# Performance work log

Hardware: AMD Instinct MI355X
Metric: run time of the kernel (lower is better)

Reference implementation:

```python
import jax, jax.numpy as jnp
import numpy as np

# Module hyperparameters (from init_kwargs)
HEAD_DIM = 64
PX = 16          # patches_x
PY = 16          # patches_y
FREQ_BASE = 100.0
FREQ_SCALE = 1.0


def _precompute_coeffs(positions):
    """RoPE cos/sin tables for one axis. feat_dim = HEAD_DIM // 2."""
    feat_dim = HEAD_DIM // 2          # each block-diagonal block is head_dim/2 wide
    num_freqs = feat_dim // 2         # rope splits block into (x, y) halves
    freqs = FREQ_SCALE * FREQ_BASE ** (-jnp.arange(num_freqs, dtype=jnp.float32) / num_freqs)
    angles = positions.astype(jnp.float32)[:, None] * freqs[None, :]   # [Sp, num_freqs]
    return jnp.cos(angles), jnp.sin(angles)


def _rope_apply(feats, cos, sin, inverse=False):
    """feats: [B, H, S, D] with D == 2*cos.shape[-1]; cos/sin: [Sp, D//2], tiled to S."""
    S = feats.shape[2]
    rep = S // cos.shape[0]           # tile per-image coeffs across cameras
    cos = jnp.tile(cos, (rep, 1))[None, None]   # [1,1,S,D//2]
    sin = jnp.tile(sin, (rep, 1))[None, None]
    d = feats.shape[-1] // 2
    x_in, y_in = feats[..., :d], feats[..., d:]
    if inverse:
        return jnp.concatenate([cos * x_in - sin * y_in, sin * x_in + cos * y_in], axis=-1)
    return jnp.concatenate([cos * x_in + sin * y_in, -sin * x_in + cos * y_in], axis=-1)


def _block_diag_rope(feats, cx, sx, cy, sy, inverse=False):
    """Block-diagonal: first head_dim//2 dims get x-axis RoPE, second half get y-axis RoPE."""
    h = feats.shape[-1] // 2
    return jnp.concatenate([
        _rope_apply(feats[..., :h], cx, sx, inverse),
        _rope_apply(feats[..., h:], cy, sy, inverse),
    ], axis=-1)


def setup_inputs() -> dict:
    key = jax.random.key(0)
    kq, kk, kv, kvm, kks = jax.random.split(key, 5)
    B, H, CAM = 2, 16, 8
    S = CAM * PX * PY   # 2048
    q = jax.random.normal(kq, (B, H, S, HEAD_DIM), dtype=jnp.float32)
    k = jax.random.normal(kk, (B, H, S, HEAD_DIM), dtype=jnp.float32)
    v = jax.random.normal(kv, (B, H, S, HEAD_DIM), dtype=jnp.float32)
    viewmats = jax.random.normal(kvm, (B, CAM, 4, 4), dtype=jnp.float32)
    Ks = jax.random.normal(kks, (B, CAM, 3, 3), dtype=jnp.float32)
    return {"q": q, "k": k, "v": v, "viewmats": viewmats, "Ks": Ks}


def reference(q, k, v, viewmats, Ks):
    # Per-image patch-grid positions, 'split' ordering: x fastest.
    pos_x = jnp.tile(jnp.arange(PX), PY)               # [PX*PY]
    pos_y = jnp.repeat(jnp.arange(PY), PX)             # [PX*PY]
    cx, sx = _precompute_coeffs(pos_x)
    cy, sy = _precompute_coeffs(pos_y)

    qe = _block_diag_rope(q, cx, sx, cy, sy)
    ke = _block_diag_rope(k, cx, sx, cy, sy)
    ve = _block_diag_rope(v, cx, sx, cy, sy)

    scale = 1.0 / jnp.sqrt(jnp.asarray(q.shape[-1], dtype=q.dtype))
    logits = jnp.einsum('bhqd,bhkd->bhqk', qe, ke) * scale
    attn = jax.nn.softmax(logits, axis=-1)
    out = jnp.einsum('bhqk,bhkd->bhqd', attn, ve)

    # Inverse RoPE on the output (PRoPE epilogue).
    return _block_diag_rope(out, cx, sx, cy, sy, inverse=True)
```

## Files before the change

kernel.cpp:

```cpp
#include <hip/hip_runtime.h>
#include <stdint.h>
#include <math.h>

typedef __attribute__((ext_vector_type(8))) short bf16x8;
typedef __attribute__((ext_vector_type(16))) float f32x16;

#define S_LEN 2048
#define D_HEAD 64
#define NT 32
#define NT_HALF 16
#define TILE_USH 4096
#define SCALE_LOG2E 0.1803368801111204f
#define M_FIXED 16.0f

static __device__ __forceinline__ unsigned short f2bf(float f) {
    union { float f; uint32_t u; } v; v.f = f;
    return (unsigned short)((v.u + 0x7fffu + ((v.u >> 16) & 1u)) >> 16);
}
static __device__ __forceinline__ uint32_t cvtpk(float lo, float hi) {
    uint32_t r;
    asm("v_cvt_pk_bf16_f32 %0, %1, %2" : "=v"(r) : "v"(lo), "v"(hi));
    return r;
}
static __device__ __forceinline__ float exp2_fast(float x) {
    float r;
    asm("v_exp_f32 %0, %1" : "=v"(r) : "v"(x));
    return r;
}
static __device__ __forceinline__ void pswap(uint32_t& a, uint32_t& b) {
    asm("v_permlane32_swap_b32 %0, %1" : "+v"(a), "+v"(b));
}

static __device__ __forceinline__ void build_tables(float (*tc)[16][16], float (*ts)[16][16],
                                                    int tid, int nthr) {
    for (int e = tid; e < 512; e += nthr) {
        int axis = e >> 8, pp = (e >> 4) & 15, j = e & 15;
        float freq = powf(100.0f, -(float)j * (1.0f / 16.0f));
        float ang = (float)pp * freq;
        float sv, cv;
        sincosf(ang, &sv, &cv);
        tc[axis][pp][j] = cv;
        ts[axis][pp][j] = sv;
    }
}

static __device__ __forceinline__ void rope_chunk(const float* __restrict__ src, int row0, int r, int c,
                                                  const float (*tc)[16][16], const float (*ts)[16][16],
                                                  float* e1, float* e2) {
    int d0 = c * 4;
    int srow = row0 + r;
    const float* p = src + (size_t)srow * D_HEAD + d0;
    float4 xv = *(const float4*)p;
    float4 yv = *(const float4*)(p + 16);
    float xs[4] = {xv.x, xv.y, xv.z, xv.w};
    float ys[4] = {yv.x, yv.y, yv.z, yv.w};
    int pos = srow & 255;
    int axis = c >> 3;
    int pp = axis ? (pos >> 4) : (pos & 15);
    int jb = d0 & 15;
#pragma unroll
    for (int i = 0; i < 4; ++i) {
        float cc = tc[axis][pp][jb + i];
        float ss = ts[axis][pp][jb + i];
        e1[i] = cc * xs[i] + ss * ys[i];
        e2[i] = cc * ys[i] - ss * xs[i];
    }
}

__global__ __launch_bounds__(256) void xyrope_prep_kernel(
    const float* __restrict__ k, const float* __restrict__ v,
    unsigned short* __restrict__ kw, unsigned short* __restrict__ vtw) {
    __shared__ unsigned short Kt[64][72];
    __shared__ unsigned short Vt[64][72];
    __shared__ float tc[2][16][16], ts[2][16][16];
    int tid = threadIdx.x;
    build_tables(tc, ts, tid, 256);
    __syncthreads();

    int bid = blockIdx.x;
    int bh = bid >> 5, kt = bid & 31;
    const float* kh = k + (size_t)bh * S_LEN * D_HEAD;
    const float* vh = v + (size_t)bh * S_LEN * D_HEAD;
    unsigned short* kimg = kw + ((size_t)bh * NT + kt) * TILE_USH;
    unsigned short* vimg = vtw + ((size_t)bh * NT + kt) * TILE_USH;

#pragma unroll
    for (int half = 0; half < 2; ++half) {
        int r = (tid >> 3) + half * 32;
        int ci_ = tid & 7;
        int c = ci_ + ((ci_ >> 2) << 2);
        int d0 = c * 4;
        float e1[4], e2[4];
        rope_chunk(kh, kt * 64, r, c, tc, ts, e1, e2);
#pragma unroll
        for (int i = 0; i < 4; ++i) { Kt[r][d0 + i] = f2bf(e1[i]); Kt[r][d0 + 16 + i] = f2bf(e2[i]); }
        rope_chunk(vh, kt * 64, r, c, tc, ts, e1, e2);
#pragma unroll
        for (int i = 0; i < 4; ++i) { Vt[r][d0 + i] = f2bf(e1[i]); Vt[r][d0 + 16 + i] = f2bf(e2[i]); }
    }
    __syncthreads();

    int l = tid & 63, grp = tid >> 6;
#pragma unroll
    for (int half = 0; half < 2; ++half) {
        int ci = grp + half * 4;
        int mt = ci & 1, ks = ci >> 1;
        {
            int row = (l & 31) + 32 * mt;
            int d0 = (l >> 5) * 8 + 16 * ks;
            uint4 w = *(const uint4*)&Kt[row][d0];
            *(uint4*)(kimg + ci * 512 + l * 8) = w;
        }
        {
            int dcol = (l & 31) + 32 * mt;
            int k0 = (l >> 5) * 8 + 16 * ks;
            union { unsigned short u[8]; uint4 q; } ov;
#pragma unroll
            for (int j = 0; j < 8; ++j) ov.u[j] = Vt[k0 + j][dcol];
            *(uint4*)(vimg + ci * 512 + l * 8) = ov.q;
        }
    }
}

struct AttnSmem {
    union {
        struct {
            unsigned short Kb[2][2][TILE_USH];
            unsigned short Vb[2][2][TILE_USH];
        } b;
        float mrg[4][64][34];
    } u;
    float tc[2][16][16];
    float ts[2][16][16];
};

static __device__ __forceinline__ void gl16(const void* g, void* l) {
    __builtin_amdgcn_global_load_lds((const __attribute__((address_space(1))) unsigned int*)g,
                                     (__attribute__((address_space(3))) unsigned int*)l, 16, 0, 0);
}
static __device__ __forceinline__ void stage_tile(const unsigned short* img, unsigned short* dstbuf, int t256) {
    const char* src = (const char*)img + t256 * 16;
    char* dst = (char*)dstbuf + (t256 >> 6) * 1024;
    gl16(src, dst);
    gl16(src + 4096, dst + 4096);
}
static __device__ __forceinline__ bf16x8 frag_ld(const unsigned short* buf, int ci, int lane) {
    union { uint4 u; bf16x8 v; } c;
    c.u = *(const uint4*)(buf + ci * 512 + lane * 8);
    return c.v;
}

__global__ __launch_bounds__(512, 4) void xyrope_attn_kernel(
    const float* __restrict__ q, const unsigned short* __restrict__ kw,
    const unsigned short* __restrict__ vtw, float* __restrict__ out) {
    __shared__ AttnSmem sm;
    int tid = threadIdx.x, bid = blockIdx.x;

    int xcd = bid & 7, slot = bid >> 3;
    int bh = xcd * 4 + (slot >> 4);
    int qt = slot & 15;

    int grp = tid >> 8;
    int t256 = tid & 255;
    const unsigned short* kimg = kw + ((size_t)bh * NT + grp * NT_HALF) * TILE_USH;
    const unsigned short* vimg = vtw + ((size_t)bh * NT + grp * NT_HALF) * TILE_USH;

    build_tables(sm.tc, sm.ts, tid, 512);
    stage_tile(kimg, sm.u.b.Kb[grp][0], t256);
    stage_tile(vimg, sm.u.b.Vb[grp][0], t256);
    __syncthreads();

    int lane = tid & 63;
    int wave = (tid >> 6) & 3;
    int ql = lane & 31, h = lane >> 5;
    int qrow = qt * 128 + wave * 32 + ql;
    int pos = qrow & 255, px = pos & 15, py = pos >> 4;

    const float* qp = q + ((size_t)bh * S_LEN + qrow) * D_HEAD + h * 8;
    float e[4][8];
#pragma unroll
    for (int ck = 0; ck < 4; ++ck) {
        float4 a = *(const float4*)(qp + ck * 16);
        float4 b = *(const float4*)(qp + ck * 16 + 4);
        e[ck][0] = a.x; e[ck][1] = a.y; e[ck][2] = a.z; e[ck][3] = a.w;
        e[ck][4] = b.x; e[ck][5] = b.y; e[ck][6] = b.z; e[ck][7] = b.w;
    }
#pragma unroll
    for (int ax = 0; ax < 2; ++ax) {
        int pp = ax ? py : px;
#pragma unroll
        for (int i = 0; i < 8; ++i) {
            float cc = sm.tc[ax][pp][8 * h + i];
            float ss = sm.ts[ax][pp][8 * h + i];
            float x = e[ax * 2][i], y = e[ax * 2 + 1][i];
            e[ax * 2][i] = (cc * x + ss * y) * SCALE_LOG2E;
            e[ax * 2 + 1][i] = (cc * y - ss * x) * SCALE_LOG2E;
        }
    }
    bf16x8 bq[4];
#pragma unroll
    for (int ck = 0; ck < 4; ++ck) {
        union { uint32_t w[4]; bf16x8 v; } uu;
#pragma unroll
        for (int t = 0; t < 4; ++t) uu.w[t] = cvtpk(e[ck][2 * t], e[ck][2 * t + 1]);
        bq[ck] = uu.v;
    }

    float l_run = 0.0f;
    f32x16 o0 = {}, o1 = {};

    for (int t = 0; t < NT_HALF; ++t) {
        int cur = t & 1;
        if (t + 1 < NT_HALF) {
            stage_tile(kimg + (t + 1) * TILE_USH, sm.u.b.Kb[grp][cur ^ 1], t256);
            stage_tile(vimg + (t + 1) * TILE_USH, sm.u.b.Vb[grp][cur ^ 1], t256);
        }
        const unsigned short* Ks = sm.u.b.Kb[grp][cur];
        const unsigned short* Vs = sm.u.b.Vb[grp][cur];

        f32x16 s0 = {}, s1 = {};
        __builtin_amdgcn_s_setprio(1);
#pragma unroll
        for (int ks = 0; ks < 4; ++ks) {
            bf16x8 a0 = frag_ld(Ks, ks * 2 + 0, lane);
            bf16x8 a1 = frag_ld(Ks, ks * 2 + 1, lane);
            s0 = __builtin_amdgcn_mfma_f32_32x32x16_bf16(a0, bq[ks], s0, 0, 0, 0);
            s1 = __builtin_amdgcn_mfma_f32_32x32x16_bf16(a1, bq[ks], s1, 0, 0, 0);
        }
        __builtin_amdgcn_s_setprio(0);

#pragma unroll
        for (int r = 0; r < 16; ++r) {
            s0[r] = exp2_fast(s0[r] - M_FIXED);
            s1[r] = exp2_fast(s1[r] - M_FIXED);
        }

        uint32_t pk[16];
#pragma unroll
        for (int tt = 0; tt < 8; ++tt) {
            pk[tt] = cvtpk(s0[2 * tt], s0[2 * tt + 1]);
            pk[8 + tt] = cvtpk(s1[2 * tt], s1[2 * tt + 1]);
        }
        float a8[8];
#pragma unroll
        for (int i = 0; i < 8; ++i)
            a8[i] = (s0[i] + s0[i + 8]) + (s1[i] + s1[i + 8]);
        l_run += ((a8[0] + a8[1]) + (a8[2] + a8[3])) + ((a8[4] + a8[5]) + (a8[6] + a8[7]));

        __builtin_amdgcn_s_setprio(1);
#pragma unroll
        for (int ks = 0; ks < 4; ++ks) {
            uint32_t w0 = pk[4 * ks], w1 = pk[4 * ks + 1], w2 = pk[4 * ks + 2], w3 = pk[4 * ks + 3];
            pswap(w0, w2);
            pswap(w1, w3);
            union { uint32_t w[4]; bf16x8 v; } pb;
            pb.w[0] = w0; pb.w[1] = w1; pb.w[2] = w2; pb.w[3] = w3;
            bf16x8 v0 = frag_ld(Vs, ks * 2 + 0, lane);
            bf16x8 v1 = frag_ld(Vs, ks * 2 + 1, lane);
            o0 = __builtin_amdgcn_mfma_f32_32x32x16_bf16(v0, pb.v, o0, 0, 0, 0);
            o1 = __builtin_amdgcn_mfma_f32_32x32x16_bf16(v1, pb.v, o1, 0, 0, 0);
        }
        __builtin_amdgcn_s_setprio(0);
        __syncthreads();
    }

    float* pl = &sm.u.mrg[wave][lane][0];
    if (grp == 1) {
#pragma unroll
        for (int r = 0; r < 16; ++r) { pl[r] = o0[r]; pl[16 + r] = o1[r]; }
        pl[32] = l_run;
    }
    __syncthreads();
    if (grp == 0) {
        float lt = l_run + pl[32];
        lt += __shfl_xor(lt, 32);
        float inv_l = 1.0f / lt;
#pragma unroll
        for (int r = 0; r < 16; ++r) {
            o0[r] += pl[r];
            o1[r] += pl[16 + r];
        }

        float* orow = out + ((size_t)bh * S_LEN + qrow) * D_HEAD;
#pragma unroll
        for (int mt = 0; mt < 2; ++mt) {
            float oo[16];
#pragma unroll
            for (int r = 0; r < 16; ++r) oo[r] = mt ? o1[r] : o0[r];
            int pp = mt ? py : px;
            float res[16];
#pragma unroll
            for (int r = 0; r < 8; ++r) {
                int j = (r & 3) + 8 * (r >> 2) + 4 * h;
                float cc = sm.tc[mt][pp][j];
                float ss = sm.ts[mt][pp][j];
                float x = oo[r] * inv_l, y = oo[r + 8] * inv_l;
                res[r] = cc * x - ss * y;
                res[r + 8] = ss * x + cc * y;
            }
#pragma unroll
            for (int gq = 0; gq < 4; ++gq) {
                float4 w = {res[gq * 4 + 0], res[gq * 4 + 1], res[gq * 4 + 2], res[gq * 4 + 3]};
                *(float4*)(orow + mt * 32 + gq * 8 + 4 * h) = w;
            }
        }
    }
}

extern "C" void kernel_launch(void* const* d_in, const int* in_sizes, int n_in,
                              void* d_out, int out_size, void* d_ws, size_t ws_size,
                              hipStream_t stream) {
    const float* q = (const float*)d_in[0];
    const float* k = (const float*)d_in[1];
    const float* v = (const float*)d_in[2];
    float* out = (float*)d_out;
    unsigned short* kw = (unsigned short*)d_ws;
    unsigned short* vtw = kw + (size_t)32 * NT * TILE_USH;
    hipLaunchKernelGGL(xyrope_prep_kernel, dim3(1024), dim3(256), 0, stream, k, v, kw, vtw);
    hipLaunchKernelGGL(xyrope_attn_kernel, dim3(512), dim3(512), 0, stream, q, kw, vtw, out);
}
```

Measured before the change: 64.99 us.

## Split key sequence across four wave groups with 32-key tiles and 1024-thread blocks

Re-layouts the prepared K and V^T images into 32-key tiles and raises the attention block to 1024 threads, so four wave groups each process a quarter of the keys instead of two groups processing halves. Each iteration now does half the MFMA work per tile, with smaller LDS staging. Partial outputs and row sums are reduced serially through shared memory across the four groups. The aim is more waves in flight to hide latency, at the cost of more barriers, a longer merge epilogue and more loop overhead per key.

```diff
diff --git a/kernel.cpp b/kernel.cpp
--- a/kernel.cpp
+++ b/kernel.cpp
@@ -7,9 +7,9 @@
 
 #define S_LEN 2048
 #define D_HEAD 64
-#define NT 32
-#define NT_HALF 16
-#define TILE_USH 4096
+#define NTILE 64
+#define TPG 16
+#define T32_USH 2048
 #define SCALE_LOG2E 0.1803368801111204f
 #define M_FIXED 16.0f
 
@@ -81,8 +81,8 @@
     int bh = bid >> 5, kt = bid & 31;
     const float* kh = k + (size_t)bh * S_LEN * D_HEAD;
     const float* vh = v + (size_t)bh * S_LEN * D_HEAD;
-    unsigned short* kimg = kw + ((size_t)bh * NT + kt) * TILE_USH;
-    unsigned short* vimg = vtw + ((size_t)bh * NT + kt) * TILE_USH;
+    unsigned short* kimg = kw + ((size_t)bh * NTILE + kt * 2) * T32_USH;
+    unsigned short* vimg = vtw + ((size_t)bh * NTILE + kt * 2) * T32_USH;
 
 #pragma unroll
     for (int half = 0; half < 2; ++half) {
@@ -100,24 +100,27 @@
     }
     __syncthreads();
 
-    int l = tid & 63, grp = tid >> 6;
-#pragma unroll
-    for (int half = 0; half < 2; ++half) {
-        int ci = grp + half * 4;
-        int mt = ci & 1, ks = ci >> 1;
+    int l = tid & 63;
+#pragma unroll
+    for (int pass = 0; pass < 2; ++pass) {
+        int g = pass * 4 + (tid >> 6);
+        int sub = g >> 2;
         {
-            int row = (l & 31) + 32 * mt;
-            int d0 = (l >> 5) * 8 + 16 * ks;
+            int ks = g & 3;
+            int row = sub * 32 + (l & 31);
+            int d0 = ks * 16 + (l >> 5) * 8;
             uint4 w = *(const uint4*)&Kt[row][d0];
-            *(uint4*)(kimg + ci * 512 + l * 8) = w;
+            *(uint4*)(kimg + (size_t)sub * T32_USH + ks * 512 + l * 8) = w;
         }
         {
+            int ci = g & 3;
+            int ks2 = ci >> 1, mt = ci & 1;
+            int k0 = sub * 32 + ks2 * 16 + (l >> 5) * 8;
             int dcol = (l & 31) + 32 * mt;
-            int k0 = (l >> 5) * 8 + 16 * ks;
             union { unsigned short u[8]; uint4 q; } ov;
 #pragma unroll
             for (int j = 0; j < 8; ++j) ov.u[j] = Vt[k0 + j][dcol];
-            *(uint4*)(vimg + ci * 512 + l * 8) = ov.q;
+            *(uint4*)(vimg + (size_t)sub * T32_USH + ci * 512 + l * 8) = ov.q;
         }
     }
 }
@@ -125,8 +128,8 @@
 struct AttnSmem {
     union {
         struct {
-            unsigned short Kb[2][2][TILE_USH];
-            unsigned short Vb[2][2][TILE_USH];
+            unsigned short Kb[4][2][T32_USH];
+            unsigned short Vb[4][2][T32_USH];
         } b;
         float mrg[4][64][34];
     } u;
@@ -142,7 +145,6 @@
     const char* src = (const char*)img + t256 * 16;
     char* dst = (char*)dstbuf + (t256 >> 6) * 1024;
     gl16(src, dst);
-    gl16(src + 4096, dst + 4096);
 }
 static __device__ __forceinline__ bf16x8 frag_ld(const unsigned short* buf, int ci, int lane) {
     union { uint4 u; bf16x8 v; } c;
@@ -150,7 +152,7 @@
     return c.v;
 }
 
-__global__ __launch_bounds__(512, 4) void xyrope_attn_kernel(
+__global__ __launch_bounds__(1024, 8) void xyrope_attn_kernel(
     const float* __restrict__ q, const unsigned short* __restrict__ kw,
     const unsigned short* __restrict__ vtw, float* __restrict__ out) {
     __shared__ AttnSmem sm;
@@ -162,18 +164,18 @@
 
     int grp = tid >> 8;
     int t256 = tid & 255;
-    const unsigned short* kimg = kw + ((size_t)bh * NT + grp * NT_HALF) * TILE_USH;
-    const unsigned short* vimg = vtw + ((size_t)bh * NT + grp * NT_HALF) * TILE_USH;
-
-    build_tables(sm.tc, sm.ts, tid, 512);
+    const unsigned short* kimg = kw + ((size_t)bh * NTILE + grp * TPG) * T32_USH;
+    const unsigned short* vimg = vtw + ((size_t)bh * NTILE + grp * TPG) * T32_USH;
+
+    build_tables(sm.tc, sm.ts, tid, 1024);
     stage_tile(kimg, sm.u.b.Kb[grp][0], t256);
     stage_tile(vimg, sm.u.b.Vb[grp][0], t256);
     __syncthreads();
 
     int lane = tid & 63;
-    int wave = (tid >> 6) & 3;
+    int qwave = (tid >> 6) & 3;
     int ql = lane & 31, h = lane >> 5;
-    int qrow = qt * 128 + wave * 32 + ql;
+    int qrow = qt * 128 + qwave * 32 + ql;
     int pos = qrow & 255, px = pos & 15, py = pos >> 4;
 
     const float* qp = q + ((size_t)bh * S_LEN + qrow) * D_HEAD + h * 8;
@@ -209,54 +211,45 @@
     float l_run = 0.0f;
     f32x16 o0 = {}, o1 = {};
 
-    for (int t = 0; t < NT_HALF; ++t) {
+    for (int t = 0; t < TPG; ++t) {
         int cur = t & 1;
-        if (t + 1 < NT_HALF) {
-            stage_tile(kimg + (t + 1) * TILE_USH, sm.u.b.Kb[grp][cur ^ 1], t256);
-            stage_tile(vimg + (t + 1) * TILE_USH, sm.u.b.Vb[grp][cur ^ 1], t256);
+        if (t + 1 < TPG) {
+            stage_tile(kimg + (t + 1) * T32_USH, sm.u.b.Kb[grp][cur ^ 1], t256);
+            stage_tile(vimg + (t + 1) * T32_USH, sm.u.b.Vb[grp][cur ^ 1], t256);
         }
         const unsigned short* Ks = sm.u.b.Kb[grp][cur];
         const unsigned short* Vs = sm.u.b.Vb[grp][cur];
 
-        f32x16 s0 = {}, s1 = {};
+        f32x16 s0 = {};
         __builtin_amdgcn_s_setprio(1);
 #pragma unroll
         for (int ks = 0; ks < 4; ++ks) {
-            bf16x8 a0 = frag_ld(Ks, ks * 2 + 0, lane);
-            bf16x8 a1 = frag_ld(Ks, ks * 2 + 1, lane);
+            bf16x8 a0 = frag_ld(Ks, ks, lane);
             s0 = __builtin_amdgcn_mfma_f32_32x32x16_bf16(a0, bq[ks], s0, 0, 0, 0);
-            s1 = __builtin_amdgcn_mfma_f32_32x32x16_bf16(a1, bq[ks], s1, 0, 0, 0);
         }
         __builtin_amdgcn_s_setprio(0);
 
 #pragma unroll
-        for (int r = 0; r < 16; ++r) {
-            s0[r] = exp2_fast(s0[r] - M_FIXED);
-            s1[r] = exp2_fast(s1[r] - M_FIXED);
-        }
-
-        uint32_t pk[16];
-#pragma unroll
-        for (int tt = 0; tt < 8; ++tt) {
-            pk[tt] = cvtpk(s0[2 * tt], s0[2 * tt + 1]);
-            pk[8 + tt] = cvtpk(s1[2 * tt], s1[2 * tt + 1]);
-        }
-        float a8[8];
-#pragma unroll
-        for (int i = 0; i < 8; ++i)
-            a8[i] = (s0[i] + s0[i + 8]) + (s1[i] + s1[i + 8]);
-        l_run += ((a8[0] + a8[1]) + (a8[2] + a8[3])) + ((a8[4] + a8[5]) + (a8[6] + a8[7]));
+        for (int r = 0; r < 16; ++r) s0[r] = exp2_fast(s0[r] - M_FIXED);
+
+        uint32_t pk[8];
+#pragma unroll
+        for (int tt = 0; tt < 8; ++tt) pk[tt] = cvtpk(s0[2 * tt], s0[2 * tt + 1]);
+        float a4[4];
+#pragma unroll
+        for (int i = 0; i < 4; ++i) a4[i] = (s0[i] + s0[i + 4]) + (s0[i + 8] + s0[i + 12]);
+        l_run += (a4[0] + a4[1]) + (a4[2] + a4[3]);
 
         __builtin_amdgcn_s_setprio(1);
 #pragma unroll
-        for (int ks = 0; ks < 4; ++ks) {
-            uint32_t w0 = pk[4 * ks], w1 = pk[4 * ks + 1], w2 = pk[4 * ks + 2], w3 = pk[4 * ks + 3];
+        for (int ks2 = 0; ks2 < 2; ++ks2) {
+            uint32_t w0 = pk[4 * ks2], w1 = pk[4 * ks2 + 1], w2 = pk[4 * ks2 + 2], w3 = pk[4 * ks2 + 3];
             pswap(w0, w2);
             pswap(w1, w3);
             union { uint32_t w[4]; bf16x8 v; } pb;
             pb.w[0] = w0; pb.w[1] = w1; pb.w[2] = w2; pb.w[3] = w3;
-            bf16x8 v0 = frag_ld(Vs, ks * 2 + 0, lane);
-            bf16x8 v1 = frag_ld(Vs, ks * 2 + 1, lane);
+            bf16x8 v0 = frag_ld(Vs, ks2 * 2 + 0, lane);
+            bf16x8 v1 = frag_ld(Vs, ks2 * 2 + 1, lane);
             o0 = __builtin_amdgcn_mfma_f32_32x32x16_bf16(v0, pb.v, o0, 0, 0, 0);
             o1 = __builtin_amdgcn_mfma_f32_32x32x16_bf16(v1, pb.v, o1, 0, 0, 0);
         }
@@ -264,11 +257,23 @@
         __syncthreads();
     }
 
-    float* pl = &sm.u.mrg[wave][lane][0];
-    if (grp == 1) {
+    float* pl = &sm.u.mrg[qwave][lane][0];
+    if (grp == 3) {
 #pragma unroll
         for (int r = 0; r < 16; ++r) { pl[r] = o0[r]; pl[16 + r] = o1[r]; }
         pl[32] = l_run;
+    }
+    __syncthreads();
+    if (grp == 2) {
+#pragma unroll
+        for (int r = 0; r < 16; ++r) { pl[r] += o0[r]; pl[16 + r] += o1[r]; }
+        pl[32] += l_run;
+    }
+    __syncthreads();
+    if (grp == 1) {
+#pragma unroll
+        for (int r = 0; r < 16; ++r) { pl[r] += o0[r]; pl[16 + r] += o1[r]; }
+        pl[32] += l_run;
     }
     __syncthreads();
     if (grp == 0) {
@@ -315,7 +320,7 @@
     const float* v = (const float*)d_in[2];
     float* out = (float*)d_out;
     unsigned short* kw = (unsigned short*)d_ws;
-    unsigned short* vtw = kw + (size_t)32 * NT * TILE_USH;
+    unsigned short* vtw = kw + (size_t)32 * NTILE * T32_USH;
     hipLaunchKernelGGL(xyrope_prep_kernel, dim3(1024), dim3(256), 0, stream, k, v, kw, vtw);
-    hipLaunchKernelGGL(xyrope_attn_kernel, dim3(512), dim3(512), 0, stream, q, kw, vtw, out);
-}
+    hipLaunchKernelGGL(xyrope_attn_kernel, dim3(512), dim3(1024), 0, stream, q, kw, vtw, out);
+}
```

New measurement: 120.8 us. +85.9%, slower.
